# Performance work log

Measured on AMD Instinct MI355X. Metric: run time of the kernel, lower is better.

The kernel has to match this reference:

```python
import jax, jax.numpy as jnp
import numpy as np

S, B, C = 7, 2, 1
LAMBDA_COORD, LAMBDA_NOOBJ = 5.0, 0.5
EPS = 1e-6
BATCH = 32768


def setup_inputs() -> dict:
    key = jax.random.key(0)
    k1, k2, k3, k4 = jax.random.split(key, 4)
    predictions = jax.random.normal(k1, (BATCH, S, S, B * 5 + C), dtype=jnp.float32)
    coords = jax.random.uniform(k2, (BATCH, S, S, 4), dtype=jnp.float32) * 0.9 + 0.05
    conf = jax.random.randint(k3, (BATCH, S, S, 1), 0, 2).astype(jnp.float32)  # exactly 0 or 1
    cls = jax.random.randint(k4, (BATCH, S, S, C), 0, 2).astype(jnp.float32)
    targets = jnp.concatenate([coords, conf, cls], axis=-1)  # [BATCH,S,S,6]
    return {"predictions": predictions, "targets": targets}


def reference(predictions, targets):
    dt = predictions.dtype
    obj = (targets[..., 4] == 1.0).astype(dt)      # [bs,S,S]
    noobj = (targets[..., 4] == 0.0).astype(dt)    # [bs,S,S]

    pb = predictions[..., : B * 5].reshape(predictions.shape[:-1] + (B, 5))  # [bs,S,S,B,5]
    tb = targets[..., :5]                                                    # [bs,S,S,5]

    # IoU of each of the B predicted boxes vs the target box (per cell)
    sxy = jax.nn.sigmoid(pb[..., 0:2])
    awh = jnp.abs(pb[..., 2:4])
    p1 = sxy - awh / 2
    p2 = sxy + awh / 2
    t1 = tb[..., 0:2] - tb[..., 2:4] / 2
    t2 = tb[..., 0:2] + tb[..., 2:4] / 2
    lo = jnp.maximum(p1, t1[..., None, :])
    hi = jnp.minimum(p2, t2[..., None, :])
    inter = jnp.prod(jnp.maximum(hi - lo, 0.0), axis=-1)        # [bs,S,S,B]
    parea = jnp.prod(jnp.abs(p2 - p1), axis=-1)                 # [bs,S,S,B]
    tarea = (tb[..., 2] * tb[..., 3])[..., None]
    iou = inter / (parea + tarea - inter + EPS)

    best = jnp.argmax(iou, axis=-1)                             # [bs,S,S]
    bb = jnp.take_along_axis(pb, best[..., None, None], axis=-2)[..., 0, :]  # [bs,S,S,5]

    coord = LAMBDA_COORD * jnp.sum(
        obj * jnp.sum((jax.nn.sigmoid(bb[..., 0:2]) - tb[..., 0:2]) ** 2, axis=-1)
    )
    coord = coord + LAMBDA_COORD * jnp.sum(
        obj * jnp.sum((jnp.sqrt(jnp.abs(bb[..., 2:4]) + EPS) - jnp.sqrt(tb[..., 2:4] + EPS)) ** 2, axis=-1)
    )

    conf_obj = jnp.sum(obj * (jax.nn.sigmoid(bb[..., 4]) - tb[..., 4]) ** 2)

    conf_noobj = LAMBDA_NOOBJ * jnp.sum(
        noobj[..., None] * (jax.nn.sigmoid(pb[..., 4]) - tb[..., 4:5]) ** 2
    )

    # C == 1: binary cross-entropy with logits, summed over obj cells
    pc = predictions[..., B * 5 : B * 5 + C]
    tc = targets[..., 5 : 5 + C]
    bce = jnp.maximum(pc, 0.0) - pc * tc + jnp.log1p(jnp.exp(-jnp.abs(pc)))
    class_loss = jnp.sum(obj[..., None] * bce)

    bs = predictions.shape[0]
    total = (coord + conf_obj + conf_noobj + class_loss) / bs
    return (total, coord / bs, conf_obj / bs, conf_noobj / bs, class_loss / bs)
```

## Files before the change

### kernel.cpp

```cpp
#include <hip/hip_runtime.h>
#include <math.h>


#define PRED_C 11
#define TGT_C  6
#define CPB    256
#define LAMBDA_COORD 5.0f
#define LAMBDA_NOOBJ 0.5f
#define EPSV 1e-6f

__device__ __forceinline__ float fsig(float x) {
    return __builtin_amdgcn_rcpf(1.0f + __expf(-x));
}

__global__ __launch_bounds__(CPB) void yolo_partial_kernel(
    const float* __restrict__ pred,
    const float* __restrict__ tgt,
    float* __restrict__ partials)
{
    __shared__ float sp[CPB * PRED_C];
    __shared__ float st[CPB * TGT_C];
    __shared__ float red[4][4];

    const int tid = threadIdx.x;
    const long long blockCell = (long long)blockIdx.x * CPB;

    {
        const float4* gp = (const float4*)(pred + blockCell * PRED_C);
        float4* lp = (float4*)sp;
        lp[tid]       = gp[tid];
        lp[tid + 256] = gp[tid + 256];
        if (tid < CPB * PRED_C / 4 - 512) lp[tid + 512] = gp[tid + 512];
        const float4* gt = (const float4*)(tgt + blockCell * TGT_C);
        float4* lt = (float4*)st;
        lt[tid] = gt[tid];
        if (tid < CPB * TGT_C / 4 - 256) lt[tid + 256] = gt[tid + 256];
    }
    __syncthreads();

    const float* p = sp + tid * PRED_C;
    const float* t = st + tid * TGT_C;

    const float tx = t[0], ty = t[1], tw = t[2], th = t[3];
    const float tconf = t[4], tcls = t[5];
    const float obj   = (tconf == 1.0f) ? 1.0f : 0.0f;
    const float noobj = (tconf == 0.0f) ? 1.0f : 0.0f;

    const float t1x = tx - tw * 0.5f, t1y = ty - th * 0.5f;
    const float t2x = tx + tw * 0.5f, t2y = ty + th * 0.5f;
    const float tarea = tw * th;

    float iou[2], sx[2], sy[2], aw[2], ah[2], scf[2];
    #pragma unroll
    for (int b = 0; b < 2; ++b) {
        sx[b]  = fsig(p[b * 5 + 0]);
        sy[b]  = fsig(p[b * 5 + 1]);
        scf[b] = fsig(p[b * 5 + 4]);
        aw[b]  = fabsf(p[b * 5 + 2]);
        ah[b]  = fabsf(p[b * 5 + 3]);
        const float p1x = sx[b] - aw[b] * 0.5f, p1y = sy[b] - ah[b] * 0.5f;
        const float p2x = sx[b] + aw[b] * 0.5f, p2y = sy[b] + ah[b] * 0.5f;
        const float ix = fminf(p2x, t2x) - fmaxf(p1x, t1x);
        const float iy = fminf(p2y, t2y) - fmaxf(p1y, t1y);
        const float inter = fmaxf(ix, 0.0f) * fmaxf(iy, 0.0f);
        const float parea = aw[b] * ah[b];
        iou[b] = inter * __builtin_amdgcn_rcpf(parea + tarea - inter + EPSV);
    }
    const int best = (iou[1] > iou[0]) ? 1 : 0;

    const float dx = sx[best] - tx;
    const float dy = sy[best] - ty;
    const float dw = __builtin_amdgcn_sqrtf(aw[best] + EPSV) -
                     __builtin_amdgcn_sqrtf(tw + EPSV);
    const float dh = __builtin_amdgcn_sqrtf(ah[best] + EPSV) -
                     __builtin_amdgcn_sqrtf(th + EPSV);
    float coord = LAMBDA_COORD * obj * ((dx * dx + dy * dy) + (dw * dw + dh * dh));

    const float sc = scf[best];
    float conf_obj = obj * (sc - tconf) * (sc - tconf);

    const float d0 = scf[0] - tconf;
    const float d1 = scf[1] - tconf;
    float conf_noobj = LAMBDA_NOOBJ * noobj * (d0 * d0 + d1 * d1);

    const float pc = p[10];
    const float bce = fmaxf(pc, 0.0f) - pc * tcls +
                      __logf(1.0f + __expf(-fabsf(pc)));
    float class_loss = obj * bce;

    #pragma unroll
    for (int off = 32; off >= 1; off >>= 1) {
        coord      += __shfl_down(coord, off);
        conf_obj   += __shfl_down(conf_obj, off);
        conf_noobj += __shfl_down(conf_noobj, off);
        class_loss += __shfl_down(class_loss, off);
    }
    const int wave = tid >> 6;
    const int lane = tid & 63;
    if (lane == 0) {
        red[wave][0] = coord;
        red[wave][1] = conf_obj;
        red[wave][2] = conf_noobj;
        red[wave][3] = class_loss;
    }
    __syncthreads();
    if (tid == 0) {
        float4 v;
        v.x = red[0][0] + red[1][0] + red[2][0] + red[3][0];
        v.y = red[0][1] + red[1][1] + red[2][1] + red[3][1];
        v.z = red[0][2] + red[1][2] + red[2][2] + red[3][2];
        v.w = red[0][3] + red[1][3] + red[2][3] + red[3][3];
        ((float4*)partials)[blockIdx.x] = v;
    }
}

__global__ __launch_bounds__(1024) void yolo_final_kernel(
    const float* __restrict__ partials,
    float* __restrict__ out,
    int nblk,
    float inv_bs)
{
    __shared__ float red[16][4];
    const int tid = threadIdx.x;

    float c = 0.f, co = 0.f, cn = 0.f, cl = 0.f;
    for (int i = tid; i < nblk; i += 1024) {
        const float4 v = ((const float4*)partials)[i];
        c += v.x; co += v.y; cn += v.z; cl += v.w;
    }
    #pragma unroll
    for (int off = 32; off >= 1; off >>= 1) {
        c  += __shfl_down(c, off);
        co += __shfl_down(co, off);
        cn += __shfl_down(cn, off);
        cl += __shfl_down(cl, off);
    }
    const int wave = tid >> 6;
    const int lane = tid & 63;
    if (lane == 0) {
        red[wave][0] = c;
        red[wave][1] = co;
        red[wave][2] = cn;
        red[wave][3] = cl;
    }
    __syncthreads();
    if (tid == 0) {
        float sc = 0.f, sco = 0.f, scn = 0.f, scl = 0.f;
        #pragma unroll
        for (int w = 0; w < 16; ++w) {
            sc  += red[w][0];
            sco += red[w][1];
            scn += red[w][2];
            scl += red[w][3];
        }
        out[0] = (sc + sco + scn + scl) * inv_bs;
        out[1] = sc  * inv_bs;
        out[2] = sco * inv_bs;
        out[3] = scn * inv_bs;
        out[4] = scl * inv_bs;
    }
}

extern "C" void kernel_launch(void* const* d_in, const int* in_sizes, int n_in,
                              void* d_out, int out_size, void* d_ws, size_t ws_size,
                              hipStream_t stream) {
    const float* pred = (const float*)d_in[0];
    const float* tgt  = (const float*)d_in[1];
    float* out = (float*)d_out;
    float* partials = (float*)d_ws;

    const long long batch = (long long)in_sizes[0] / (7 * 7 * PRED_C);
    const long long cells = batch * 49;
    const int nblk = (int)(cells / CPB);

    yolo_partial_kernel<<<nblk, CPB, 0, stream>>>(pred, tgt, partials);
    yolo_final_kernel<<<1, 1024, 0, stream>>>(partials, out, nblk,
                                              1.0f / (float)batch);
}
```

Measured before the change: 134.0 us.

## Double-buffer tiles via async global-to-LDS loads with multiple tiles per block

New measurement: 131.1 us. -2.2%, faster.

```diff
diff --git a/kernel.cpp b/kernel.cpp
--- a/kernel.cpp
+++ b/kernel.cpp
@@ -4,104 +4,128 @@
 
 #define PRED_C 11
 #define TGT_C  6
-#define CPB    256
+#define TPB    256
+#define TILES_PER_BLOCK 4
 #define LAMBDA_COORD 5.0f
 #define LAMBDA_NOOBJ 0.5f
 #define EPSV 1e-6f
 
+typedef unsigned int u32;
+
+__device__ __forceinline__ void gll16(const float* g, float* l) {
+    __builtin_amdgcn_global_load_lds(
+        (const __attribute__((address_space(1))) u32*)g,
+        (__attribute__((address_space(3))) u32*)l,
+        16, 0, 0);
+}
+
 __device__ __forceinline__ float fsig(float x) {
     return __builtin_amdgcn_rcpf(1.0f + __expf(-x));
 }
 
-__global__ __launch_bounds__(CPB) void yolo_partial_kernel(
+__global__ __launch_bounds__(TPB) void yolo_partial_kernel(
     const float* __restrict__ pred,
     const float* __restrict__ tgt,
-    float* __restrict__ partials)
+    float* __restrict__ partials,
+    int ntiles)
 {
-    __shared__ float sp[CPB * PRED_C];
-    __shared__ float st[CPB * TGT_C];
+    __shared__ __align__(16) float sp[2][TPB * PRED_C];
+    __shared__ __align__(16) float st[2][TPB * TGT_C];
     __shared__ float red[4][4];
 
     const int tid = threadIdx.x;
-    const long long blockCell = (long long)blockIdx.x * CPB;
-
-    {
-        const float4* gp = (const float4*)(pred + blockCell * PRED_C);
-        float4* lp = (float4*)sp;
-        lp[tid]       = gp[tid];
-        lp[tid + 256] = gp[tid + 256];
-        if (tid < CPB * PRED_C / 4 - 512) lp[tid + 512] = gp[tid + 512];
-        const float4* gt = (const float4*)(tgt + blockCell * TGT_C);
-        float4* lt = (float4*)st;
-        lt[tid] = gt[tid];
-        if (tid < CPB * TGT_C / 4 - 256) lt[tid + 256] = gt[tid + 256];
-    }
+    const int wv  = tid >> 6;
+    const int ln  = tid & 63;
+
+    auto stage = [&](int t, int b) {
+        const float* pbase = pred + (long long)t * (TPB * PRED_C);
+        const float* tbase = tgt  + (long long)t * (TPB * TGT_C);
+        #pragma unroll
+        for (int o = wv; o < 17; o += 4) {
+            if (o < 11) gll16(pbase + o * 256 + ln * 4, &sp[b][o * 256]);
+            else        gll16(tbase + (o - 11) * 256 + ln * 4, &st[b][(o - 11) * 256]);
+        }
+    };
+
+    float acc_coord = 0.f, acc_cobj = 0.f, acc_cnoobj = 0.f, acc_cls = 0.f;
+
+    int tile = blockIdx.x;
+    stage(tile, 0);
     __syncthreads();
 
-    const float* p = sp + tid * PRED_C;
-    const float* t = st + tid * TGT_C;
-
-    const float tx = t[0], ty = t[1], tw = t[2], th = t[3];
-    const float tconf = t[4], tcls = t[5];
-    const float obj   = (tconf == 1.0f) ? 1.0f : 0.0f;
-    const float noobj = (tconf == 0.0f) ? 1.0f : 0.0f;
-
-    const float t1x = tx - tw * 0.5f, t1y = ty - th * 0.5f;
-    const float t2x = tx + tw * 0.5f, t2y = ty + th * 0.5f;
-    const float tarea = tw * th;
-
-    float iou[2], sx[2], sy[2], aw[2], ah[2], scf[2];
+    int cur = 0;
     #pragma unroll
-    for (int b = 0; b < 2; ++b) {
-        sx[b]  = fsig(p[b * 5 + 0]);
-        sy[b]  = fsig(p[b * 5 + 1]);
-        scf[b] = fsig(p[b * 5 + 4]);
-        aw[b]  = fabsf(p[b * 5 + 2]);
-        ah[b]  = fabsf(p[b * 5 + 3]);
-        const float p1x = sx[b] - aw[b] * 0.5f, p1y = sy[b] - ah[b] * 0.5f;
-        const float p2x = sx[b] + aw[b] * 0.5f, p2y = sy[b] + ah[b] * 0.5f;
-        const float ix = fminf(p2x, t2x) - fmaxf(p1x, t1x);
-        const float iy = fminf(p2y, t2y) - fmaxf(p1y, t1y);
-        const float inter = fmaxf(ix, 0.0f) * fmaxf(iy, 0.0f);
-        const float parea = aw[b] * ah[b];
-        iou[b] = inter * __builtin_amdgcn_rcpf(parea + tarea - inter + EPSV);
-    }
-    const int best = (iou[1] > iou[0]) ? 1 : 0;
-
-    const float dx = sx[best] - tx;
-    const float dy = sy[best] - ty;
-    const float dw = __builtin_amdgcn_sqrtf(aw[best] + EPSV) -
-                     __builtin_amdgcn_sqrtf(tw + EPSV);
-    const float dh = __builtin_amdgcn_sqrtf(ah[best] + EPSV) -
-                     __builtin_amdgcn_sqrtf(th + EPSV);
-    float coord = LAMBDA_COORD * obj * ((dx * dx + dy * dy) + (dw * dw + dh * dh));
-
-    const float sc = scf[best];
-    float conf_obj = obj * (sc - tconf) * (sc - tconf);
-
-    const float d0 = scf[0] - tconf;
-    const float d1 = scf[1] - tconf;
-    float conf_noobj = LAMBDA_NOOBJ * noobj * (d0 * d0 + d1 * d1);
-
-    const float pc = p[10];
-    const float bce = fmaxf(pc, 0.0f) - pc * tcls +
-                      __logf(1.0f + __expf(-fabsf(pc)));
-    float class_loss = obj * bce;
+    for (int i = 0; i < TILES_PER_BLOCK; ++i) {
+        const int tn = tile + gridDim.x;
+        if (i < TILES_PER_BLOCK - 1 && tn < ntiles) stage(tn, cur ^ 1);
+
+        const float* p = &sp[cur][tid * PRED_C];
+        const float* t = &st[cur][tid * TGT_C];
+
+        const float tx = t[0], ty = t[1], tw = t[2], th = t[3];
+        const float tconf = t[4], tcls = t[5];
+        const float obj   = (tconf == 1.0f) ? 1.0f : 0.0f;
+        const float noobj = (tconf == 0.0f) ? 1.0f : 0.0f;
+
+        const float t1x = tx - tw * 0.5f, t1y = ty - th * 0.5f;
+        const float t2x = tx + tw * 0.5f, t2y = ty + th * 0.5f;
+        const float tarea = tw * th;
+
+        float iou[2], sx[2], sy[2], aw[2], ah[2], scf[2];
+        #pragma unroll
+        for (int b = 0; b < 2; ++b) {
+            sx[b]  = fsig(p[b * 5 + 0]);
+            sy[b]  = fsig(p[b * 5 + 1]);
+            scf[b] = fsig(p[b * 5 + 4]);
+            aw[b]  = fabsf(p[b * 5 + 2]);
+            ah[b]  = fabsf(p[b * 5 + 3]);
+            const float p1x = sx[b] - aw[b] * 0.5f, p1y = sy[b] - ah[b] * 0.5f;
+            const float p2x = sx[b] + aw[b] * 0.5f, p2y = sy[b] + ah[b] * 0.5f;
+            const float ix = fminf(p2x, t2x) - fmaxf(p1x, t1x);
+            const float iy = fminf(p2y, t2y) - fmaxf(p1y, t1y);
+            const float inter = fmaxf(ix, 0.0f) * fmaxf(iy, 0.0f);
+            const float parea = aw[b] * ah[b];
+            iou[b] = inter * __builtin_amdgcn_rcpf(parea + tarea - inter + EPSV);
+        }
+        const int best = (iou[1] > iou[0]) ? 1 : 0;
+
+        const float dx = sx[best] - tx;
+        const float dy = sy[best] - ty;
+        const float dw = __builtin_amdgcn_sqrtf(aw[best] + EPSV) -
+                         __builtin_amdgcn_sqrtf(tw + EPSV);
+        const float dh = __builtin_amdgcn_sqrtf(ah[best] + EPSV) -
+                         __builtin_amdgcn_sqrtf(th + EPSV);
+        acc_coord += LAMBDA_COORD * obj * ((dx * dx + dy * dy) + (dw * dw + dh * dh));
+
+        const float sc = scf[best];
+        acc_cobj += obj * (sc - tconf) * (sc - tconf);
+
+        const float d0 = scf[0] - tconf;
+        const float d1 = scf[1] - tconf;
+        acc_cnoobj += LAMBDA_NOOBJ * noobj * (d0 * d0 + d1 * d1);
+
+        const float pc = p[10];
+        const float bce = fmaxf(pc, 0.0f) - pc * tcls +
+                          __logf(1.0f + __expf(-fabsf(pc)));
+        acc_cls += obj * bce;
+
+        __syncthreads();
+        cur ^= 1;
+        tile = tn;
+    }
 
     #pragma unroll
     for (int off = 32; off >= 1; off >>= 1) {
-        coord      += __shfl_down(coord, off);
-        conf_obj   += __shfl_down(conf_obj, off);
-        conf_noobj += __shfl_down(conf_noobj, off);
-        class_loss += __shfl_down(class_loss, off);
-    }
-    const int wave = tid >> 6;
-    const int lane = tid & 63;
-    if (lane == 0) {
-        red[wave][0] = coord;
-        red[wave][1] = conf_obj;
-        red[wave][2] = conf_noobj;
-        red[wave][3] = class_loss;
+        acc_coord  += __shfl_down(acc_coord, off);
+        acc_cobj   += __shfl_down(acc_cobj, off);
+        acc_cnoobj += __shfl_down(acc_cnoobj, off);
+        acc_cls    += __shfl_down(acc_cls, off);
+    }
+    if (ln == 0) {
+        red[wv][0] = acc_coord;
+        red[wv][1] = acc_cobj;
+        red[wv][2] = acc_cnoobj;
+        red[wv][3] = acc_cls;
     }
     __syncthreads();
     if (tid == 0) {
@@ -171,9 +195,10 @@
 
     const long long batch = (long long)in_sizes[0] / (7 * 7 * PRED_C);
     const long long cells = batch * 49;
-    const int nblk = (int)(cells / CPB);
-
-    yolo_partial_kernel<<<nblk, CPB, 0, stream>>>(pred, tgt, partials);
+    const int ntiles = (int)(cells / TPB);
+    const int nblk = ntiles / TILES_PER_BLOCK;
+
+    yolo_partial_kernel<<<nblk, TPB, 0, stream>>>(pred, tgt, partials, ntiles);
     yolo_final_kernel<<<1, 1024, 0, stream>>>(partials, out, nblk,
                                               1.0f / (float)batch);
 }
```
